# Optimization experiments

Measured on AMD Instinct MI355X. Metric: run time of the kernel, lower is better.

Reference implementation:

```python
import jax, jax.numpy as jnp
import numpy as np

NUM_CLASSES = 1000
FEAT_DIM = 512
BATCH = 16384


def setup_inputs() -> dict:
    key = jax.random.key(0)
    k1, k2, k3 = jax.random.split(key, 3)
    x = jax.random.normal(k1, (BATCH, FEAT_DIM), dtype=jnp.float32)
    labels = jax.random.randint(k2, (BATCH,), 0, NUM_CLASSES, dtype=jnp.int64)
    centers = jax.random.normal(k3, (NUM_CLASSES, FEAT_DIM), dtype=jnp.float32)
    margin = jnp.ones((1,), dtype=jnp.float32)
    return {"x": x, "labels": labels, "centers": centers, "margin": margin}


def reference(x, labels, centers, margin):
    # squared euclidean distances: [B, C]
    distmat = (
        jnp.sum(x * x, axis=1, keepdims=True)
        + jnp.sum(centers * centers, axis=1)[None, :]
        - 2.0 * (x @ centers.T)
    )
    B, C = distmat.shape
    onehot = labels[:, None] == jnp.arange(C, dtype=labels.dtype)[None, :]  # [B, C]
    # distance to the true-class center
    dist = jnp.sum(jnp.where(onehot, distmat, 0.0), axis=1)  # [B]
    # min distance over all other classes (mask true class with +inf)
    dist_min = jnp.min(jnp.where(onehot, jnp.inf, distmat), axis=1)  # [B]
    m = margin[0]
    loss = jnp.sum(jnp.maximum(m + dist - dist_min, 0.0)) / B
    return loss
```

## Files before the change

kernel.cpp:

```cpp
#include <hip/hip_runtime.h>
#include <hip/hip_bf16.h>

#define BATCH 16384
#define NCLS  1000
#define NPAD  1024
#define FDIM  512

#define CBLK_STRIDE 266240
#define TAIL_OFF    262144

typedef __bf16 bf16x4 __attribute__((ext_vector_type(4)));
typedef __bf16 bf16x8 __attribute__((ext_vector_type(8)));
typedef float  f32x16 __attribute__((ext_vector_type(16)));

#define GLOBAL_AS __attribute__((address_space(1)))
#define LDS_AS    __attribute__((address_space(3)))

#define VMCNT(n) asm volatile("s_waitcnt vmcnt(" #n ")" ::: "memory")
#define LGKM0()  asm volatile("s_waitcnt lgkmcnt(0)" ::: "memory")
#define BAR()    do { LGKM0(); __builtin_amdgcn_s_barrier(); \
                      __builtin_amdgcn_sched_barrier(0); } while (0)

__global__ __launch_bounds__(64) void prep_centers(
    const float* __restrict__ centers, char* __restrict__ cbt,
    float* __restrict__ out)
{
    const int c = blockIdx.x, t = threadIdx.x;
    const int cblk = c >> 8, cl = c & 255;
    char* base = cbt + (size_t)cblk * CBLK_STRIDE;
    if (c == 0 && t == 0) out[0] = 0.f;

    float4 f0 = make_float4(0.f, 0.f, 0.f, 0.f);
    float4 f1 = make_float4(0.f, 0.f, 0.f, 0.f);
    if (c < NCLS) {
        f0 = *(const float4*)(centers + (size_t)c * FDIM + t * 8);
        f1 = *(const float4*)(centers + (size_t)c * FDIM + t * 8 + 4);
    }
    bf16x8 b;
    b[0] = (__bf16)f0.x; b[1] = (__bf16)f0.y; b[2] = (__bf16)f0.z; b[3] = (__bf16)f0.w;
    b[4] = (__bf16)f1.x; b[5] = (__bf16)f1.y; b[6] = (__bf16)f1.z; b[7] = (__bf16)f1.w;
    *(bf16x8*)(base + (t >> 3) * 32768 + (t & 7) * 4096 + cl * 16) = b;

    float ssum = f0.x*f0.x + f0.y*f0.y + f0.z*f0.z + f0.w*f0.w
               + f1.x*f1.x + f1.y*f1.y + f1.z*f1.z + f1.w*f1.w;
    #pragma unroll
    for (int o = 32; o > 0; o >>= 1) ssum += __shfl_down(ssum, o);
    if (t == 0) {
        const float hf = (c < NCLS) ? (-0.5f * ssum) : -1e30f;
        const __bf16 h = (__bf16)hf;
        const __bf16 l = (c < NCLS) ? (__bf16)(hf - (float)h) : (__bf16)0.f;
        bf16x8 tl;
        #pragma unroll
        for (int e = 0; e < 8; ++e) tl[e] = (__bf16)0.f;
        tl[0] = h; tl[1] = l;
        *(bf16x8*)(base + TAIL_OFF + cl * 16) = tl;
    }
}

struct B8 { float4 a, b, c, d, e, f, g, h; };

__global__ __launch_bounds__(512, 1) void trip_main(
    const float* __restrict__ x, const int* __restrict__ labels,
    const char* __restrict__ cbt, float* __restrict__ mxp,
    float* __restrict__ dap)
{
    extern __shared__ char lds[];
    const int t    = threadIdx.x;
    const int lane = t & 63;
    const int w    = t >> 6;
    const int wN   = w & 3, wM = w >> 2;
    const int l31  = lane & 31, hi = lane >> 5;
    const int bid  = blockIdx.x;
    const int cblk = bid >> 6;
    const int bblk = bid & 63;
    const int class0 = cblk * 256;
    const int row0   = bblk * 256;
    const char* cbB  = cbt + (size_t)cblk * CBLK_STRIDE;

    auto stageA = [&](int ko, int ai) {
        const char* src = cbB + ko * 32768 + t * 16;
        char* dst = lds + ai * 32768 + t * 16;
        #pragma unroll
        for (int j = 0; j < 4; ++j)
            __builtin_amdgcn_global_load_lds(
                (const GLOBAL_AS void*)(src + j * 8192),
                (LDS_AS void*)(dst + j * 8192), 16, 0, 0);
    };
    auto loadB = [&](int ko, B8& br) {
        const float* src = x + (size_t)(row0 + w * 32 + (lane >> 3)) * FDIM
                         + ko * 64 + (lane & 7) * 4;
        br.a = *(const float4*)(src);
        br.b = *(const float4*)(src + 32);
        br.c = *(const float4*)(src +  8 * FDIM);
        br.d = *(const float4*)(src +  8 * FDIM + 32);
        br.e = *(const float4*)(src + 16 * FDIM);
        br.f = *(const float4*)(src + 16 * FDIM + 32);
        br.g = *(const float4*)(src + 24 * FDIM);
        br.h = *(const float4*)(src + 24 * FDIM + 32);
    };
    auto cv4 = [](float4 f) {
        bf16x4 v;
        v[0] = (__bf16)f.x; v[1] = (__bf16)f.y;
        v[2] = (__bf16)f.z; v[3] = (__bf16)f.w;
        return v;
    };
    auto writeB = [&](const B8& br, int bi) {
        char* dst = lds + 65536 + bi * 32768 + ((lane & 7) >> 1) * 4096
                  + (w * 32 + (lane >> 3)) * 16 + (lane & 1) * 8;
        *(bf16x4*)(dst              ) = cv4(br.a);
        *(bf16x4*)(dst + 4 * 4096   ) = cv4(br.b);
        *(bf16x4*)(dst + 128        ) = cv4(br.c);
        *(bf16x4*)(dst + 4 * 4096 + 128) = cv4(br.d);
        *(bf16x4*)(dst + 256        ) = cv4(br.e);
        *(bf16x4*)(dst + 4 * 4096 + 256) = cv4(br.f);
        *(bf16x4*)(dst + 384        ) = cv4(br.g);
        *(bf16x4*)(dst + 4 * 4096 + 384) = cv4(br.h);
    };

    f32x16 acc[4][2];
    #pragma unroll
    for (int mi = 0; mi < 4; ++mi)
        #pragma unroll
        for (int ni = 0; ni < 2; ++ni)
            #pragma unroll
            for (int r = 0; r < 16; ++r) acc[mi][ni][r] = 0.f;

    auto compute = [&](int buf) {
        const char* A = lds + buf * 32768;
        const char* B = lds + 65536 + buf * 32768;
        #pragma unroll
        for (int ks = 0; ks < 4; ++ks) {
            const int chunk = ks * 2 + hi;
            bf16x8 a[4], b[2];
            #pragma unroll
            for (int mi = 0; mi < 4; ++mi)
                a[mi] = *(const bf16x8*)(A + chunk * 4096 + (wM * 128 + mi * 32 + l31) * 16);
            #pragma unroll
            for (int ni = 0; ni < 2; ++ni)
                b[ni] = *(const bf16x8*)(B + chunk * 4096 + (wN * 64 + ni * 32 + l31) * 16);
            #pragma unroll
            for (int mi = 0; mi < 4; ++mi)
                #pragma unroll
                for (int ni = 0; ni < 2; ++ni)
                    acc[mi][ni] = __builtin_amdgcn_mfma_f32_32x32x16_bf16(
                        a[mi], b[ni], acc[mi][ni], 0, 0, 0);
        }
    };

    const int lab0 = labels[row0 + wN * 64 + l31];
    const int lab1 = labels[row0 + wN * 64 + 32 + l31];
    if (t < 256) {
        const char* src = cbB + TAIL_OFF + t * 16;
        char* dst = lds + 131072 + t * 16;
        __builtin_amdgcn_global_load_lds((const GLOBAL_AS void*)src,
                                         (LDS_AS void*)dst, 16, 0, 0);
    }
    B8 brA, brB;
    stageA(0, 0); loadB(0, brA);
    __builtin_amdgcn_sched_barrier(0);
    loadB(1, brB); stageA(1, 1);
    VMCNT(12);
    writeB(brA, 0);
    BAR();

    #pragma unroll
    for (int tt = 0; tt < 8; ++tt) {
        if (tt >= 1 && tt <= 6) stageA(tt + 1, (tt + 1) & 1);
        if (tt <= 5) {
            if (tt & 1) loadB(tt + 2, brB);
            else        loadB(tt + 2, brA);
        }
        if (tt <= 5)      VMCNT(12);
        else if (tt == 6) VMCNT(4);
        else              VMCNT(0);
        if (tt <= 6) {
            if (tt & 1) writeB(brA, (tt + 1) & 1);
            else        writeB(brB, (tt + 1) & 1);
        }
        compute(tt & 1);
        BAR();
    }

    {
        const char* T = lds + 131072;
        bf16x8 bt;
        #pragma unroll
        for (int e = 0; e < 8; ++e) bt[e] = (__bf16)0.f;
        if (hi == 0) { bt[0] = (__bf16)1.0f; bt[1] = (__bf16)1.0f; }
        #pragma unroll
        for (int mi = 0; mi < 4; ++mi) {
            bf16x8 a = *(const bf16x8*)(T + (wM * 128 + mi * 32 + l31) * 16);
            #pragma unroll
            for (int ni = 0; ni < 2; ++ni)
                acc[mi][ni] = __builtin_amdgcn_mfma_f32_32x32x16_bf16(
                    a, bt, acc[mi][ni], 0, 0, 0);
        }
    }

    const int labBase = class0 + wM * 128 + hi * 4;
    const int labA0 = lab0 - labBase;
    const int labA1 = lab1 - labBase;
    float MX0 = -3e38f, MX1 = -3e38f, DA0 = -3e38f, DA1 = -3e38f;
    #pragma unroll
    for (int mi = 0; mi < 4; ++mi) {
        #pragma unroll
        for (int r = 0; r < 16; ++r) {
            const int pat = mi * 32 + (r & 3) + 8 * (r >> 2);
            {
                const float a = acc[mi][0][r];
                const bool is = (labA0 == pat);
                MX0 = fmaxf(MX0, is ? -3e38f : a);
                DA0 = is ? a : DA0;
            }
            {
                const float a = acc[mi][1][r];
                const bool is = (labA1 == pat);
                MX1 = fmaxf(MX1, is ? -3e38f : a);
                DA1 = is ? a : DA1;
            }
        }
    }
    MX0 = fmaxf(MX0, __shfl_xor(MX0, 32));
    DA0 = fmaxf(DA0, __shfl_xor(DA0, 32));
    MX1 = fmaxf(MX1, __shfl_xor(MX1, 32));
    DA1 = fmaxf(DA1, __shfl_xor(DA1, 32));

    float* sc = (float*)(lds + 65536);
    const int i0 = (wN * 2 + 0) * 32 + l31;
    const int i1 = (wN * 2 + 1) * 32 + l31;
    if (wM == 1 && hi == 0) {
        sc[i0] = MX0; sc[256 + i0] = DA0;
        sc[i1] = MX1; sc[256 + i1] = DA1;
    }
    __syncthreads();
    if (wM == 0 && hi == 0) {
        const float M0 = fmaxf(MX0, sc[i0]),  D0 = fmaxf(DA0, sc[256 + i0]);
        const float M1 = fmaxf(MX1, sc[i1]),  D1 = fmaxf(DA1, sc[256 + i1]);
        const int rg = row0 + wN * 64 + l31;
        mxp[cblk * BATCH + rg]      = M0;
        dap[cblk * BATCH + rg]      = D0;
        mxp[cblk * BATCH + rg + 32] = M1;
        dap[cblk * BATCH + rg + 32] = D1;
    }
}

__global__ __launch_bounds__(256) void combine(
    const float* __restrict__ mxp, const float* __restrict__ dap,
    const float* __restrict__ margin, float* __restrict__ out)
{
    const int t = threadIdx.x;
    const int row = blockIdx.x * 256 + t;
    float mx = fmaxf(fmaxf(mxp[row], mxp[BATCH + row]),
                     fmaxf(mxp[2 * BATCH + row], mxp[3 * BATCH + row]));
    float da = fmaxf(fmaxf(dap[row], dap[BATCH + row]),
                     fmaxf(dap[2 * BATCH + row], dap[3 * BATCH + row]));
    float loss = fmaxf(margin[0] - 2.f * da + 2.f * mx, 0.f);
    __shared__ float red[4];
    #pragma unroll
    for (int o = 32; o > 0; o >>= 1) loss += __shfl_down(loss, o);
    if ((t & 63) == 0) red[t >> 6] = loss;
    __syncthreads();
    if (t == 0)
        atomicAdd(out, (red[0] + red[1] + red[2] + red[3]) * (1.0f / BATCH));
}

extern "C" void kernel_launch(void* const* d_in, const int* in_sizes, int n_in,
                              void* d_out, int out_size, void* d_ws, size_t ws_size,
                              hipStream_t stream)
{
    const float* x       = (const float*)d_in[0];
    const int*   labels  = (const int*)d_in[1];
    const float* centers = (const float*)d_in[2];
    const float* margin  = (const float*)d_in[3];
    float* out = (float*)d_out;

    char* ws = (char*)d_ws;
    char*  cbt  = ws;
    float* mxp  = (float*)(ws + 1064960);
    float* dap  = (float*)(ws + 1327104);

    (void)hipFuncSetAttribute((const void*)trip_main,
                              hipFuncAttributeMaxDynamicSharedMemorySize, 135168);

    prep_centers<<<NPAD, 64, 0, stream>>>(centers, cbt, out);
    trip_main<<<256, 512, 135168, stream>>>(x, labels, cbt, mxp, dap);
    combine<<<64, 256, 0, stream>>>(mxp, dap, margin, out);
}
```

Measured before the change: 33.95 us.

## Interleave global loads and LDS writes across MFMA phases with ping-pong barriers

Restructures the main K loop into four sub-phases per tile. Each phase loads A/B fragments from LDS, then issues one slice of the next tile's global staging (A stage, B lo, B hi, or B write), then runs 8 MFMAs at raised wave priority, with barriers around each compute cluster. The aim is to spread memory issue across compute and keep waves in lockstep, so MFMA and memory work overlap better. It adds many more barriers per iteration, and the changed vmcnt accounting (stageA for tile 1 moved into the loop) risks ordering mistakes.

```diff
diff --git a/kernel.cpp b/kernel.cpp
--- a/kernel.cpp
+++ b/kernel.cpp
@@ -18,8 +18,8 @@
 
 #define VMCNT(n) asm volatile("s_waitcnt vmcnt(" #n ")" ::: "memory")
 #define LGKM0()  asm volatile("s_waitcnt lgkmcnt(0)" ::: "memory")
-#define BAR()    do { LGKM0(); __builtin_amdgcn_s_barrier(); \
-                      __builtin_amdgcn_sched_barrier(0); } while (0)
+#define SBAR()   __builtin_amdgcn_s_barrier()
+#define SCHED0() __builtin_amdgcn_sched_barrier(0)
 
 __global__ __launch_bounds__(64) void prep_centers(
     const float* __restrict__ centers, char* __restrict__ cbt,
@@ -86,13 +86,17 @@
                 (const GLOBAL_AS void*)(src + j * 8192),
                 (LDS_AS void*)(dst + j * 8192), 16, 0, 0);
     };
-    auto loadB = [&](int ko, B8& br) {
+    auto loadB_lo = [&](int ko, B8& br) {
         const float* src = x + (size_t)(row0 + w * 32 + (lane >> 3)) * FDIM
                          + ko * 64 + (lane & 7) * 4;
         br.a = *(const float4*)(src);
         br.b = *(const float4*)(src + 32);
         br.c = *(const float4*)(src +  8 * FDIM);
         br.d = *(const float4*)(src +  8 * FDIM + 32);
+    };
+    auto loadB_hi = [&](int ko, B8& br) {
+        const float* src = x + (size_t)(row0 + w * 32 + (lane >> 3)) * FDIM
+                         + ko * 64 + (lane & 7) * 4;
         br.e = *(const float4*)(src + 16 * FDIM);
         br.f = *(const float4*)(src + 16 * FDIM + 32);
         br.g = *(const float4*)(src + 24 * FDIM);
@@ -107,13 +111,13 @@
     auto writeB = [&](const B8& br, int bi) {
         char* dst = lds + 65536 + bi * 32768 + ((lane & 7) >> 1) * 4096
                   + (w * 32 + (lane >> 3)) * 16 + (lane & 1) * 8;
-        *(bf16x4*)(dst              ) = cv4(br.a);
-        *(bf16x4*)(dst + 4 * 4096   ) = cv4(br.b);
-        *(bf16x4*)(dst + 128        ) = cv4(br.c);
+        *(bf16x4*)(dst                 ) = cv4(br.a);
+        *(bf16x4*)(dst + 4 * 4096      ) = cv4(br.b);
+        *(bf16x4*)(dst + 128           ) = cv4(br.c);
         *(bf16x4*)(dst + 4 * 4096 + 128) = cv4(br.d);
-        *(bf16x4*)(dst + 256        ) = cv4(br.e);
+        *(bf16x4*)(dst + 256           ) = cv4(br.e);
         *(bf16x4*)(dst + 4 * 4096 + 256) = cv4(br.f);
-        *(bf16x4*)(dst + 384        ) = cv4(br.g);
+        *(bf16x4*)(dst + 384           ) = cv4(br.g);
         *(bf16x4*)(dst + 4 * 4096 + 384) = cv4(br.h);
     };
 
@@ -124,28 +128,6 @@
         for (int ni = 0; ni < 2; ++ni)
             #pragma unroll
             for (int r = 0; r < 16; ++r) acc[mi][ni][r] = 0.f;
-
-    auto compute = [&](int buf) {
-        const char* A = lds + buf * 32768;
-        const char* B = lds + 65536 + buf * 32768;
-        #pragma unroll
-        for (int ks = 0; ks < 4; ++ks) {
-            const int chunk = ks * 2 + hi;
-            bf16x8 a[4], b[2];
-            #pragma unroll
-            for (int mi = 0; mi < 4; ++mi)
-                a[mi] = *(const bf16x8*)(A + chunk * 4096 + (wM * 128 + mi * 32 + l31) * 16);
-            #pragma unroll
-            for (int ni = 0; ni < 2; ++ni)
-                b[ni] = *(const bf16x8*)(B + chunk * 4096 + (wN * 64 + ni * 32 + l31) * 16);
-            #pragma unroll
-            for (int mi = 0; mi < 4; ++mi)
-                #pragma unroll
-                for (int ni = 0; ni < 2; ++ni)
-                    acc[mi][ni] = __builtin_amdgcn_mfma_f32_32x32x16_bf16(
-                        a[mi], b[ni], acc[mi][ni], 0, 0, 0);
-        }
-    };
 
     const int lab0 = labels[row0 + wN * 64 + l31];
     const int lab1 = labels[row0 + wN * 64 + 32 + l31];
@@ -156,29 +138,61 @@
                                          (LDS_AS void*)dst, 16, 0, 0);
     }
     B8 brA, brB;
-    stageA(0, 0); loadB(0, brA);
-    __builtin_amdgcn_sched_barrier(0);
-    loadB(1, brB); stageA(1, 1);
-    VMCNT(12);
+    stageA(0, 0);
+    loadB_lo(0, brA); loadB_hi(0, brA);
+    SCHED0();
+    loadB_lo(1, brB); loadB_hi(1, brB);
+    VMCNT(8);
     writeB(brA, 0);
-    BAR();
+    LGKM0(); SBAR(); SCHED0();
 
     #pragma unroll
     for (int tt = 0; tt < 8; ++tt) {
-        if (tt >= 1 && tt <= 6) stageA(tt + 1, (tt + 1) & 1);
-        if (tt <= 5) {
-            if (tt & 1) loadB(tt + 2, brB);
-            else        loadB(tt + 2, brA);
+        const int cur = tt & 1, oth = cur ^ 1;
+        const char* A  = lds + cur * 32768;
+        const char* Bb = lds + 65536 + cur * 32768;
+        #pragma unroll
+        for (int p = 0; p < 4; ++p) {
+            if (p == 3) {
+                if (tt <= 5)      VMCNT(8);
+                else if (tt == 6) VMCNT(0);
+            }
+            const int chunk = p * 2 + hi;
+            bf16x8 a0 = *(const bf16x8*)(A + chunk * 4096 + (wM * 128 +  0 + l31) * 16);
+            bf16x8 a1 = *(const bf16x8*)(A + chunk * 4096 + (wM * 128 + 32 + l31) * 16);
+            bf16x8 a2 = *(const bf16x8*)(A + chunk * 4096 + (wM * 128 + 64 + l31) * 16);
+            bf16x8 a3 = *(const bf16x8*)(A + chunk * 4096 + (wM * 128 + 96 + l31) * 16);
+            bf16x8 b0 = *(const bf16x8*)(Bb + chunk * 4096 + (wN * 64 +  0 + l31) * 16);
+            bf16x8 b1 = *(const bf16x8*)(Bb + chunk * 4096 + (wN * 64 + 32 + l31) * 16);
+            if (p == 0 && tt < 7) stageA(tt + 1, oth);
+            if (p == 1 && tt <= 5) {
+                if (tt & 1) loadB_lo(tt + 2, brB);
+                else        loadB_lo(tt + 2, brA);
+            }
+            if (p == 2 && tt <= 5) {
+                if (tt & 1) loadB_hi(tt + 2, brB);
+                else        loadB_hi(tt + 2, brA);
+            }
+            if (p == 3 && tt <= 6) {
+                if (tt & 1) writeB(brA, oth);
+                else        writeB(brB, oth);
+            }
+            SBAR();
+            LGKM0();
+            SCHED0();
+            __builtin_amdgcn_s_setprio(1);
+            acc[0][0] = __builtin_amdgcn_mfma_f32_32x32x16_bf16(a0, b0, acc[0][0], 0, 0, 0);
+            acc[0][1] = __builtin_amdgcn_mfma_f32_32x32x16_bf16(a0, b1, acc[0][1], 0, 0, 0);
+            acc[1][0] = __builtin_amdgcn_mfma_f32_32x32x16_bf16(a1, b0, acc[1][0], 0, 0, 0);
+            acc[1][1] = __builtin_amdgcn_mfma_f32_32x32x16_bf16(a1, b1, acc[1][1], 0, 0, 0);
+            acc[2][0] = __builtin_amdgcn_mfma_f32_32x32x16_bf16(a2, b0, acc[2][0], 0, 0, 0);
+            acc[2][1] = __builtin_amdgcn_mfma_f32_32x32x16_bf16(a2, b1, acc[2][1], 0, 0, 0);
+            acc[3][0] = __builtin_amdgcn_mfma_f32_32x32x16_bf16(a3, b0, acc[3][0], 0, 0, 0);
+            acc[3][1] = __builtin_amdgcn_mfma_f32_32x32x16_bf16(a3, b1, acc[3][1], 0, 0, 0);
+            __builtin_amdgcn_s_setprio(0);
+            SBAR();
+            SCHED0();
         }
-        if (tt <= 5)      VMCNT(12);
-        else if (tt == 6) VMCNT(4);
-        else              VMCNT(0);
-        if (tt <= 6) {
-            if (tt & 1) writeB(brA, (tt + 1) & 1);
-            else        writeB(brB, (tt + 1) & 1);
-        }
-        compute(tt & 1);
-        BAR();
     }
 
     {
```

Measured after the change: 35.71 us. +5.2%, slower.

## Halve row tile and K-step to run two GEMM blocks per CU

Applied to the files above, without the earlier changes.

The main fused distance GEMM now uses 256x128 block tiles with a K-step of 32 instead of 256x256 tiles with a K-step of 64. The center repacking layout and the LDS buffers shrink to match, and the grid doubles to 512 blocks. Launch bounds now permit several resident blocks per CU, so one block's loads can overlap another block's compute. In exchange, each block reuses less data, runs twice as many loop iterations and barriers, and the center tile load now waits right after issue instead of being prefetched a step ahead. The final per-row reduction across the four warp rows now goes through LDS in a single pass.

```diff
diff --git a/kernel.cpp b/kernel.cpp
--- a/kernel.cpp
+++ b/kernel.cpp
@@ -39,7 +39,7 @@
     bf16x8 b;
     b[0] = (__bf16)f0.x; b[1] = (__bf16)f0.y; b[2] = (__bf16)f0.z; b[3] = (__bf16)f0.w;
     b[4] = (__bf16)f1.x; b[5] = (__bf16)f1.y; b[6] = (__bf16)f1.z; b[7] = (__bf16)f1.w;
-    *(bf16x8*)(base + (t >> 3) * 32768 + (t & 7) * 4096 + cl * 16) = b;
+    *(bf16x8*)(base + (t >> 2) * 16384 + (t & 3) * 4096 + cl * 16) = b;
 
     float ssum = f0.x*f0.x + f0.y*f0.y + f0.z*f0.z + f0.w*f0.w
                + f1.x*f1.x + f1.y*f1.y + f1.z*f1.z + f1.w*f1.w;
@@ -57,9 +57,9 @@
     }
 }
 
-struct B8 { float4 a, b, c, d, e, f, g, h; };
-
-__global__ __launch_bounds__(512, 1) void trip_main(
+struct B2 { float4 a, b; };
+
+__global__ __launch_bounds__(512, 4) void trip_main(
     const float* __restrict__ x, const int* __restrict__ labels,
     const char* __restrict__ cbt, float* __restrict__ mxp,
     float* __restrict__ dap)
@@ -68,35 +68,28 @@
     const int t    = threadIdx.x;
     const int lane = t & 63;
     const int w    = t >> 6;
-    const int wN   = w & 3, wM = w >> 2;
+    const int wM   = w >> 1, wN = w & 1;
     const int l31  = lane & 31, hi = lane >> 5;
     const int bid  = blockIdx.x;
-    const int cblk = bid >> 6;
-    const int bblk = bid & 63;
+    const int cblk = bid >> 7;
+    const int bblk = bid & 127;
     const int class0 = cblk * 256;
-    const int row0   = bblk * 256;
+    const int row0   = bblk * 128;
     const char* cbB  = cbt + (size_t)cblk * CBLK_STRIDE;
 
     auto stageA = [&](int ko, int ai) {
-        const char* src = cbB + ko * 32768 + t * 16;
-        char* dst = lds + ai * 32768 + t * 16;
-        #pragma unroll
-        for (int j = 0; j < 4; ++j)
-            __builtin_amdgcn_global_load_lds(
-                (const GLOBAL_AS void*)(src + j * 8192),
-                (LDS_AS void*)(dst + j * 8192), 16, 0, 0);
-    };
-    auto loadB = [&](int ko, B8& br) {
-        const float* src = x + (size_t)(row0 + w * 32 + (lane >> 3)) * FDIM
-                         + ko * 64 + (lane & 7) * 4;
+        const char* src = cbB + ko * 16384 + t * 16;
+        char* dst = lds + ai * 16384 + t * 16;
+        __builtin_amdgcn_global_load_lds((const GLOBAL_AS void*)src,
+                                         (LDS_AS void*)dst, 16, 0, 0);
+        __builtin_amdgcn_global_load_lds((const GLOBAL_AS void*)(src + 8192),
+                                         (LDS_AS void*)(dst + 8192), 16, 0, 0);
+    };
+    auto loadB = [&](int ko, B2& br) {
+        const float* src = x + (size_t)(row0 + w * 16 + (lane >> 3)) * FDIM
+                         + ko * 32 + (lane & 7) * 4;
         br.a = *(const float4*)(src);
-        br.b = *(const float4*)(src + 32);
-        br.c = *(const float4*)(src +  8 * FDIM);
-        br.d = *(const float4*)(src +  8 * FDIM + 32);
-        br.e = *(const float4*)(src + 16 * FDIM);
-        br.f = *(const float4*)(src + 16 * FDIM + 32);
-        br.g = *(const float4*)(src + 24 * FDIM);
-        br.h = *(const float4*)(src + 24 * FDIM + 32);
+        br.b = *(const float4*)(src + 8 * FDIM);
     };
     auto cv4 = [](float4 f) {
         bf16x4 v;
@@ -104,46 +97,35 @@
         v[2] = (__bf16)f.z; v[3] = (__bf16)f.w;
         return v;
     };
-    auto writeB = [&](const B8& br, int bi) {
-        char* dst = lds + 65536 + bi * 32768 + ((lane & 7) >> 1) * 4096
-                  + (w * 32 + (lane >> 3)) * 16 + (lane & 1) * 8;
-        *(bf16x4*)(dst              ) = cv4(br.a);
-        *(bf16x4*)(dst + 4 * 4096   ) = cv4(br.b);
-        *(bf16x4*)(dst + 128        ) = cv4(br.c);
-        *(bf16x4*)(dst + 4 * 4096 + 128) = cv4(br.d);
-        *(bf16x4*)(dst + 256        ) = cv4(br.e);
-        *(bf16x4*)(dst + 4 * 4096 + 256) = cv4(br.f);
-        *(bf16x4*)(dst + 384        ) = cv4(br.g);
-        *(bf16x4*)(dst + 4 * 4096 + 384) = cv4(br.h);
-    };
-
-    f32x16 acc[4][2];
-    #pragma unroll
-    for (int mi = 0; mi < 4; ++mi)
+    auto writeB = [&](const B2& br, int bi) {
+        char* dst = lds + 32768 + bi * 8192 + ((lane & 7) >> 1) * 2048
+                  + (w * 16 + (lane >> 3)) * 16 + (lane & 1) * 8;
+        *(bf16x4*)(dst      ) = cv4(br.a);
+        *(bf16x4*)(dst + 128) = cv4(br.b);
+    };
+
+    f32x16 acc[2][2];
+    #pragma unroll
+    for (int mi = 0; mi < 2; ++mi)
         #pragma unroll
         for (int ni = 0; ni < 2; ++ni)
             #pragma unroll
             for (int r = 0; r < 16; ++r) acc[mi][ni][r] = 0.f;
 
     auto compute = [&](int buf) {
-        const char* A = lds + buf * 32768;
-        const char* B = lds + 65536 + buf * 32768;
-        #pragma unroll
-        for (int ks = 0; ks < 4; ++ks) {
+        const char* A = lds + buf * 16384;
+        const char* B = lds + 32768 + buf * 8192;
+        #pragma unroll
+        for (int ks = 0; ks < 2; ++ks) {
             const int chunk = ks * 2 + hi;
-            bf16x8 a[4], b[2];
-            #pragma unroll
-            for (int mi = 0; mi < 4; ++mi)
-                a[mi] = *(const bf16x8*)(A + chunk * 4096 + (wM * 128 + mi * 32 + l31) * 16);
-            #pragma unroll
-            for (int ni = 0; ni < 2; ++ni)
-                b[ni] = *(const bf16x8*)(B + chunk * 4096 + (wN * 64 + ni * 32 + l31) * 16);
-            #pragma unroll
-            for (int mi = 0; mi < 4; ++mi)
-                #pragma unroll
-                for (int ni = 0; ni < 2; ++ni)
-                    acc[mi][ni] = __builtin_amdgcn_mfma_f32_32x32x16_bf16(
-                        a[mi], b[ni], acc[mi][ni], 0, 0, 0);
+            bf16x8 a0 = *(const bf16x8*)(A + chunk * 4096 + (wM * 64 +  0 + l31) * 16);
+            bf16x8 a1 = *(const bf16x8*)(A + chunk * 4096 + (wM * 64 + 32 + l31) * 16);
+            bf16x8 b0 = *(const bf16x8*)(B + chunk * 2048 + (wN * 64 +  0 + l31) * 16);
+            bf16x8 b1 = *(const bf16x8*)(B + chunk * 2048 + (wN * 64 + 32 + l31) * 16);
+            acc[0][0] = __builtin_amdgcn_mfma_f32_32x32x16_bf16(a0, b0, acc[0][0], 0, 0, 0);
+            acc[0][1] = __builtin_amdgcn_mfma_f32_32x32x16_bf16(a0, b1, acc[0][1], 0, 0, 0);
+            acc[1][0] = __builtin_amdgcn_mfma_f32_32x32x16_bf16(a1, b0, acc[1][0], 0, 0, 0);
+            acc[1][1] = __builtin_amdgcn_mfma_f32_32x32x16_bf16(a1, b1, acc[1][1], 0, 0, 0);
         }
     };
 
@@ -151,45 +133,45 @@
     const int lab1 = labels[row0 + wN * 64 + 32 + l31];
     if (t < 256) {
         const char* src = cbB + TAIL_OFF + t * 16;
-        char* dst = lds + 131072 + t * 16;
+        char* dst = lds + 49152 + t * 16;
         __builtin_amdgcn_global_load_lds((const GLOBAL_AS void*)src,
                                          (LDS_AS void*)dst, 16, 0, 0);
     }
-    B8 brA, brB;
+    B2 brA, brB;
     stageA(0, 0); loadB(0, brA);
     __builtin_amdgcn_sched_barrier(0);
-    loadB(1, brB); stageA(1, 1);
-    VMCNT(12);
+    loadB(1, brB);
+    VMCNT(2);
     writeB(brA, 0);
     BAR();
 
     #pragma unroll
-    for (int tt = 0; tt < 8; ++tt) {
-        if (tt >= 1 && tt <= 6) stageA(tt + 1, (tt + 1) & 1);
-        if (tt <= 5) {
+    for (int tt = 0; tt < 16; ++tt) {
+        const int cur = tt & 1, oth = cur ^ 1;
+        if (tt < 15) stageA(tt + 1, oth);
+        if (tt <= 13) {
             if (tt & 1) loadB(tt + 2, brB);
             else        loadB(tt + 2, brA);
         }
-        if (tt <= 5)      VMCNT(12);
-        else if (tt == 6) VMCNT(4);
-        else              VMCNT(0);
-        if (tt <= 6) {
-            if (tt & 1) writeB(brA, (tt + 1) & 1);
-            else        writeB(brB, (tt + 1) & 1);
-        }
-        compute(tt & 1);
+        if (tt <= 13)      VMCNT(2);
+        else if (tt == 14) VMCNT(0);
+        if (tt <= 14) {
+            if (tt & 1) writeB(brA, oth);
+            else        writeB(brB, oth);
+        }
+        compute(cur);
         BAR();
     }
 
     {
-        const char* T = lds + 131072;
+        const char* T = lds + 49152;
         bf16x8 bt;
         #pragma unroll
         for (int e = 0; e < 8; ++e) bt[e] = (__bf16)0.f;
         if (hi == 0) { bt[0] = (__bf16)1.0f; bt[1] = (__bf16)1.0f; }
         #pragma unroll
-        for (int mi = 0; mi < 4; ++mi) {
-            bf16x8 a = *(const bf16x8*)(T + (wM * 128 + mi * 32 + l31) * 16);
+        for (int mi = 0; mi < 2; ++mi) {
+            bf16x8 a = *(const bf16x8*)(T + (wM * 64 + mi * 32 + l31) * 16);
             #pragma unroll
             for (int ni = 0; ni < 2; ++ni)
                 acc[mi][ni] = __builtin_amdgcn_mfma_f32_32x32x16_bf16(
@@ -197,12 +179,12 @@
         }
     }
 
-    const int labBase = class0 + wM * 128 + hi * 4;
+    const int labBase = class0 + wM * 64 + hi * 4;
     const int labA0 = lab0 - labBase;
     const int labA1 = lab1 - labBase;
     float MX0 = -3e38f, MX1 = -3e38f, DA0 = -3e38f, DA1 = -3e38f;
     #pragma unroll
-    for (int mi = 0; mi < 4; ++mi) {
+    for (int mi = 0; mi < 2; ++mi) {
         #pragma unroll
         for (int r = 0; r < 16; ++r) {
             const int pat = mi * 32 + (r & 3) + 8 * (r >> 2);
@@ -225,22 +207,22 @@
     MX1 = fmaxf(MX1, __shfl_xor(MX1, 32));
     DA1 = fmaxf(DA1, __shfl_xor(DA1, 32));
 
-    float* sc = (float*)(lds + 65536);
-    const int i0 = (wN * 2 + 0) * 32 + l31;
-    const int i1 = (wN * 2 + 1) * 32 + l31;
-    if (wM == 1 && hi == 0) {
-        sc[i0] = MX0; sc[256 + i0] = DA0;
-        sc[i1] = MX1; sc[256 + i1] = DA1;
-    }
+    float* scm = (float*)lds;
+    float* scd = scm + 512;
     __syncthreads();
-    if (wM == 0 && hi == 0) {
-        const float M0 = fmaxf(MX0, sc[i0]),  D0 = fmaxf(DA0, sc[256 + i0]);
-        const float M1 = fmaxf(MX1, sc[i1]),  D1 = fmaxf(DA1, sc[256 + i1]);
-        const int rg = row0 + wN * 64 + l31;
-        mxp[cblk * BATCH + rg]      = M0;
-        dap[cblk * BATCH + rg]      = D0;
-        mxp[cblk * BATCH + rg + 32] = M1;
-        dap[cblk * BATCH + rg + 32] = D1;
+    if (hi == 0) {
+        const int r0 = wN * 64 + l31;
+        scm[wM * 128 + r0]      = MX0;  scd[wM * 128 + r0]      = DA0;
+        scm[wM * 128 + r0 + 32] = MX1;  scd[wM * 128 + r0 + 32] = DA1;
+    }
+    __syncthreads();
+    if (t < 128) {
+        const float mx = fmaxf(fmaxf(scm[t], scm[128 + t]),
+                               fmaxf(scm[256 + t], scm[384 + t]));
+        const float da = fmaxf(fmaxf(scd[t], scd[128 + t]),
+                               fmaxf(scd[256 + t], scd[384 + t]));
+        mxp[cblk * BATCH + row0 + t] = mx;
+        dap[cblk * BATCH + row0 + t] = da;
     }
 }
 
@@ -280,9 +262,9 @@
     float* dap  = (float*)(ws + 1327104);
 
     (void)hipFuncSetAttribute((const void*)trip_main,
-                              hipFuncAttributeMaxDynamicSharedMemorySize, 135168);
+                              hipFuncAttributeMaxDynamicSharedMemorySize, 53248);
 
     prep_centers<<<NPAD, 64, 0, stream>>>(centers, cbt, out);
-    trip_main<<<256, 512, 135168, stream>>>(x, labels, cbt, mxp, dap);
+    trip_main<<<512, 512, 53248, stream>>>(x, labels, cbt, mxp, dap);
     combine<<<64, 256, 0, stream>>>(mxp, dap, margin, out);
 }
```

Result: faster. 33.18 us, median of 2 (-2.3%).
